# Kernel tuning notes

Hardware: AMD Instinct MI355X
Metric: run time of the kernel (lower is better)

The kernel has to match this reference:

```python
import jax, jax.numpy as jnp
import numpy as np

B, S, E = 4, 1024, 1024
H = 16
HD = E // H  # 64
NEXP = 8
FF = 4 * E
EPS = 1e-5


def _ln(x, g, b):
    m = jnp.mean(x, axis=-1, keepdims=True)
    v = jnp.var(x, axis=-1, keepdims=True)
    return (x - m) * jax.lax.rsqrt(v + EPS) * g + b


def setup_inputs() -> dict:
    key = jax.random.key(0)
    ks = jax.random.split(key, 16)
    sd = 0.02
    inp = {
        "x": jax.random.normal(ks[0], (B, S, E), jnp.float32),
        # per-head Q/K/V linears, stacked over heads: [H, E, HD]
        "wq": jax.random.normal(ks[1], (H, E, HD), jnp.float32) * sd,
        "bq": jnp.zeros((H, HD), jnp.float32),
        "wk": jax.random.normal(ks[2], (H, E, HD), jnp.float32) * sd,
        "bk": jnp.zeros((H, HD), jnp.float32),
        "wv": jax.random.normal(ks[3], (H, E, HD), jnp.float32) * sd,
        "bv": jnp.zeros((H, HD), jnp.float32),
        "wp": jax.random.normal(ks[4], (E, E), jnp.float32) * sd,
        "bp": jnp.zeros((E,), jnp.float32),
        "ln1_g": jnp.ones((E,), jnp.float32),
        "ln1_b": jnp.zeros((E,), jnp.float32),
        "ln2_g": jnp.ones((E,), jnp.float32),
        "ln2_b": jnp.zeros((E,), jnp.float32),
        "wr": jax.random.normal(ks[5], (E, NEXP), jnp.float32) * sd,
        "br": jnp.zeros((NEXP,), jnp.float32),
        # experts stacked: [NEXP, E, FF], [NEXP, FF, E]
        "w1": jax.random.normal(ks[6], (NEXP, E, FF), jnp.float32) * sd,
        "b1": jnp.zeros((NEXP, FF), jnp.float32),
        "w2": jax.random.normal(ks[7], (NEXP, FF, E), jnp.float32) * sd,
        "b2": jnp.zeros((NEXP, E), jnp.float32),
    }
    return inp


def _block(x, wq, bq, wk, bk, wv, bv, wp, bp, ln1_g, ln1_b, ln2_g, ln2_b,
           wr, br, w1, b1, w2, b2):
    # --- multi-head causal attention (per-head Q/K/V, concat, project) ---
    q = jnp.einsum('bse,hed->bhsd', x, wq) + bq[None, :, None, :]
    k = jnp.einsum('bse,hed->bhsd', x, wk) + bk[None, :, None, :]
    v = jnp.einsum('bse,hed->bhsd', x, wv) + bv[None, :, None, :]
    scores = jnp.einsum('bhsd,bhtd->bhst', q, k) / jnp.sqrt(jnp.float32(HD))
    causal = jnp.tril(jnp.ones((S, S), bool))
    scores = jnp.where(causal[None, None], scores, -jnp.inf)
    attn = jax.nn.softmax(scores, axis=-1)
    heads = jnp.einsum('bhst,bhtd->bhsd', attn, v)
    # concat heads (dim order matches torch.cat over head list)
    cat = heads.transpose(0, 2, 1, 3).reshape(B, S, E)
    attn_out = cat @ wp + bp
    # --- residual + LN1 ---
    h = _ln(attn_out + x, ln1_g, ln1_b)
    # --- MoE: router probs weight ALL experts densely (indices unused) ---
    probs = jax.nn.softmax(h @ wr + br, axis=-1)  # [B,S,NEXP]
    mid = jax.nn.relu(jnp.einsum('bse,nef->bnsf', h, w1) + b1[None, :, None, :])
    eo = jnp.einsum('bnsf,nfe->bnse', mid, w2) + b2[None, :, None, :]
    moe_out = jnp.einsum('bnse,bsn->bse', eo, probs)
    # --- residual uses ORIGINAL inputs (as in source) + LN2 ---
    return _ln(moe_out + x, ln2_g, ln2_b)


def reference(x, wq, bq, wk, bk, wv, bv, wp, bp, ln1_g, ln1_b, ln2_g, ln2_b,
              wr, br, w1, b1, w2, b2):
    return _block(x, wq, bq, wk, bk, wv, bv, wp, bp, ln1_g, ln1_b,
                  ln2_g, ln2_b, wr, br, w1, b1, w2, b2)
```

## Files before the change

kernel.cpp:

```cpp
#include <hip/hip_runtime.h>
#include <hip/hip_bf16.h>

typedef unsigned short u16;
typedef unsigned int u32;
typedef __attribute__((ext_vector_type(8))) short bf16x8;
typedef __attribute__((ext_vector_type(4))) float f32x4;

#define DEV static __device__ __forceinline__

DEV u16 f2b(float f) {
  union { float f; u32 u; } v; v.f = f;
  return (u16)((v.u + 0x7fffu + ((v.u >> 16) & 1u)) >> 16);
}

DEV void gload16(const void* g, void* l) {
  __builtin_amdgcn_global_load_lds(
      (const __attribute__((address_space(1))) u32*)g,
      (__attribute__((address_space(3))) u32*)l, 16, 0, 0);
}

__global__ __launch_bounds__(256) void cvt_bf16(const float* __restrict__ s,
                                                u16* __restrict__ d) {
  const long i = ((long)blockIdx.x * 256 + threadIdx.x) * 4;
  const float4 v = *(const float4*)&s[i];
  ushort4 o;
  o.x = f2b(v.x); o.y = f2b(v.y); o.z = f2b(v.z); o.w = f2b(v.w);
  *(ushort4*)&d[i] = o;
}

__global__ __launch_bounds__(256) void tpose_bf16(const float* __restrict__ src,
                                                  u16* __restrict__ dst, int R,
                                                  int C, long sStride,
                                                  long dStride) {
  __shared__ float tl[32][33];
  const float* s = src + (long)blockIdx.z * sStride;
  u16* d = dst + (long)blockIdx.z * dStride;
  const int c0 = blockIdx.x * 32, r0 = blockIdx.y * 32;
  const int tx = threadIdx.x, ty = threadIdx.y;
#pragma unroll
  for (int k = 0; k < 4; k++)
    tl[ty + k * 8][tx] = s[(long)(r0 + ty + k * 8) * C + c0 + tx];
  __syncthreads();
#pragma unroll
  for (int k = 0; k < 4; k++)
    d[(long)(c0 + ty + k * 8) * R + r0 + tx] = f2b(tl[tx][ty + k * 8]);
}

enum { EQKV, EPROJ, EFF1, EFF2, EFF2I };

template <int EPI>
__global__ __launch_bounds__(256, 2) void gemm_bt(
    const u16* __restrict__ A, const u16* __restrict__ Bt, int K, int lda,
    int ldb, const float* __restrict__ c0, const float* __restrict__ c1,
    const float* __restrict__ c2, const float* __restrict__ aux,
    float* __restrict__ fout, u16* __restrict__ o0, u16* __restrict__ o1,
    u16* __restrict__ o2, int nexp) {
  __shared__ u16 As[4096], Bs[4096];
  if constexpr (EPI == EFF2 || EPI == EFF2I) {
    const int z = blockIdx.z;
    A += (long)z * 2048;
    Bt += (long)z * 2048;
    fout += (long)z * 4194304;
  }
  const int tid = threadIdx.x;
  const int m0 = blockIdx.y * 128, n0 = blockIdx.x * 128;
  const int w = tid >> 6, l = tid & 63;
  const int wm = (w >> 1) * 64, wn = (w & 1) * 64;
  const int lr = l & 15, lh = l >> 4;
  f32x4 acc[4][4] = {};
  const u16* Ag = A + (long)(m0 + (tid >> 2)) * lda + (tid & 3) * 8;
  const u16* Bg = Bt + (long)(n0 + (tid >> 2)) * ldb + (tid & 3) * 8;
  const long rsA = (long)64 * lda, rsB = (long)64 * ldb;
  for (int kt = 0; kt < K; kt += 32) {
    __syncthreads();
    gload16(Ag, As + tid * 8);
    gload16(Ag + rsA, As + tid * 8 + 2048);
    gload16(Bg, Bs + tid * 8);
    gload16(Bg + rsB, Bs + tid * 8 + 2048);
    Ag += 32; Bg += 32;
    __syncthreads();
    bf16x8 af[4], bfr[4];
#pragma unroll
    for (int i = 0; i < 4; i++)
      af[i] = *(const bf16x8*)&As[(wm + i * 16 + lr) * 32 + lh * 8];
#pragma unroll
    for (int j = 0; j < 4; j++)
      bfr[j] = *(const bf16x8*)&Bs[(wn + j * 16 + lr) * 32 + lh * 8];
#pragma unroll
    for (int i = 0; i < 4; i++)
#pragma unroll
      for (int j = 0; j < 4; j++)
        acc[i][j] = __builtin_amdgcn_mfma_f32_16x16x32_bf16(af[i], bfr[j],
                                                            acc[i][j], 0, 0, 0);
  }
#pragma unroll
  for (int j = 0; j < 4; j++) {
    const int col = n0 + wn + j * 16 + lr;
#pragma unroll
    for (int i = 0; i < 4; i++)
#pragma unroll
      for (int r = 0; r < 4; r++) {
        const int row = m0 + wm + i * 16 + lh * 4 + r;
        float v = acc[i][j][r];
        if constexpr (EPI == EQKV) {
          const int which = col >> 10, hd = col & 1023;
          const float vb =
              v + ((which == 0) ? c0 : (which == 1) ? c1 : c2)[hd];
          const int b = row >> 10, s = row & 1023;
          const int h = hd >> 6, d = hd & 63;
          const long bh = b * 16 + h;
          if (which == 0)
            o0[(bh * 1024 + s) * 64 + d] = f2b(vb * 0.125f);
          else if (which == 1)
            o1[(bh * 1024 + s) * 64 + d] = f2b(vb);
          else
            o2[bh * 65536 + (long)d * 1024 + s] = f2b(vb);
        } else if constexpr (EPI == EPROJ) {
          const long idx = (long)row * 1024 + col;
          fout[idx] = v + c0[col] + aux[idx];
        } else if constexpr (EPI == EFF1) {
          const float t = v + c0[col];
          o0[(long)row * 4096 + col] = f2b(t > 0.f ? t : 0.f);
        } else {
          float vb = v;
          if (blockIdx.z == 0) vb += c0[col];
          const float t = aux[row * 8 + nexp] * vb;
          const long idx = (long)row * 1024 + col;
          if constexpr (EPI == EFF2I)
            fout[idx] = t;
          else
            fout[idx] = fout[idx] + t;
        }
      }
  }
}

__global__ __launch_bounds__(256) void attn_fwd(const u16* __restrict__ Qb,
                                                const u16* __restrict__ Kb,
                                                const u16* __restrict__ Vt,
                                                u16* __restrict__ Cat) {
  __shared__ u16 Pl[4][512];
  const int tid = threadIdx.x;
  const int w = tid >> 6, l = tid & 63;
  const int lr = l & 15, lh = l >> 4;
  const int bh = blockIdx.y;
  const int q0 = blockIdx.x * 64 + w * 16;
  const u16* Qp = Qb + (long)bh * 65536;
  const u16* Kp = Kb + (long)bh * 65536;
  const u16* Vp = Vt + (long)bh * 65536;
  const bf16x8 qf0 = *(const bf16x8*)&Qp[(q0 + lr) * 64 + lh * 8];
  const bf16x8 qf1 = *(const bf16x8*)&Qp[(q0 + lr) * 64 + 32 + lh * 8];
  f32x4 o[4] = {};
  float mrow[4] = {-1e30f, -1e30f, -1e30f, -1e30f};
  float ssum[4] = {0.f, 0.f, 0.f, 0.f};
  u16* P = Pl[w];
  const int nkt = (q0 + 15) / 32 + 1;
  for (int kt = 0; kt < nkt; kt++) {
    const int t0 = kt * 32;
    f32x4 sc[2];
#pragma unroll
    for (int ts = 0; ts < 2; ts++) {
      const bf16x8 kf0 =
          *(const bf16x8*)&Kp[(t0 + ts * 16 + lr) * 64 + lh * 8];
      const bf16x8 kf1 =
          *(const bf16x8*)&Kp[(t0 + ts * 16 + lr) * 64 + 32 + lh * 8];
      f32x4 c = {};
      c = __builtin_amdgcn_mfma_f32_16x16x32_bf16(qf0, kf0, c, 0, 0, 0);
      c = __builtin_amdgcn_mfma_f32_16x16x32_bf16(qf1, kf1, c, 0, 0, 0);
      sc[ts] = c;
    }
#pragma unroll
    for (int ts = 0; ts < 2; ts++) {
      const int tcol = t0 + ts * 16 + lr;
#pragma unroll
      for (int i = 0; i < 4; i++)
        if (tcol > q0 + lh * 4 + i) sc[ts][i] = -1e30f;
    }
    float mt[4], mnew[4], scl[4], ps[4];
#pragma unroll
    for (int i = 0; i < 4; i++) mt[i] = fmaxf(sc[0][i], sc[1][i]);
#pragma unroll
    for (int d = 1; d < 16; d <<= 1)
#pragma unroll
      for (int i = 0; i < 4; i++) mt[i] = fmaxf(mt[i], __shfl_xor(mt[i], d));
#pragma unroll
    for (int i = 0; i < 4; i++) {
      mnew[i] = fmaxf(mrow[i], mt[i]);
      scl[i] = __expf(mrow[i] - mnew[i]);
      mrow[i] = mnew[i];
      ps[i] = 0.f;
    }
#pragma unroll
    for (int ts = 0; ts < 2; ts++)
#pragma unroll
      for (int i = 0; i < 4; i++) {
        const float p = __expf(sc[ts][i] - mnew[i]);
        ps[i] += p;
        P[(lh * 4 + i) * 32 + ts * 16 + lr] = f2b(p);
      }
#pragma unroll
    for (int d = 1; d < 16; d <<= 1)
#pragma unroll
      for (int i = 0; i < 4; i++) ps[i] += __shfl_xor(ps[i], d);
#pragma unroll
    for (int i = 0; i < 4; i++) ssum[i] = ssum[i] * scl[i] + ps[i];
#pragma unroll
    for (int dt = 0; dt < 4; dt++)
#pragma unroll
      for (int i = 0; i < 4; i++) o[dt][i] *= scl[i];
    const bf16x8 pf = *(const bf16x8*)&P[lr * 32 + lh * 8];
#pragma unroll
    for (int dt = 0; dt < 4; dt++) {
      const bf16x8 vf =
          *(const bf16x8*)&Vp[(dt * 16 + lr) * 1024 + t0 + lh * 8];
      o[dt] = __builtin_amdgcn_mfma_f32_16x16x32_bf16(pf, vf, o[dt], 0, 0, 0);
    }
  }
  const int b = bh >> 4, h = bh & 15;
#pragma unroll
  for (int dt = 0; dt < 4; dt++)
#pragma unroll
    for (int i = 0; i < 4; i++) {
      const int q = q0 + lh * 4 + i;
      Cat[((long)(b * 1024 + q)) * 1024 + h * 64 + dt * 16 + lr] =
          f2b(o[dt][i] / ssum[i]);
    }
}

DEV float wred(float v) {
#pragma unroll
  for (int d = 1; d < 64; d <<= 1) v += __shfl_xor(v, d);
  return v;
}

__global__ __launch_bounds__(256) void ln1_router(
    const float* __restrict__ in, const float* __restrict__ g,
    const float* __restrict__ bb, const float* __restrict__ wr,
    const float* __restrict__ br, u16* __restrict__ h,
    float* __restrict__ probs) {
  __shared__ float rs[4], rs2[4], rp[4][8];
  const int row = blockIdx.x, t = threadIdx.x;
  const int w = t >> 6, l = t & 63;
  const float4 v = *(const float4*)&in[(long)row * 1024 + t * 4];
  float s = v.x + v.y + v.z + v.w;
  float s2 = v.x * v.x + v.y * v.y + v.z * v.z + v.w * v.w;
  s = wred(s);
  s2 = wred(s2);
  if (l == 0) { rs[w] = s; rs2[w] = s2; }
  __syncthreads();
  const float S = rs[0] + rs[1] + rs[2] + rs[3];
  const float S2 = rs2[0] + rs2[1] + rs2[2] + rs2[3];
  const float mean = S * (1.f / 1024.f);
  const float var = S2 * (1.f / 1024.f) - mean * mean;
  const float rr = rsqrtf(var + 1e-5f);
  const float4 gv = *(const float4*)&g[t * 4];
  const float4 bv = *(const float4*)&bb[t * 4];
  float hv[4];
  hv[0] = (v.x - mean) * rr * gv.x + bv.x;
  hv[1] = (v.y - mean) * rr * gv.y + bv.y;
  hv[2] = (v.z - mean) * rr * gv.z + bv.z;
  hv[3] = (v.w - mean) * rr * gv.w + bv.w;
  ushort4 hb;
  hb.x = f2b(hv[0]); hb.y = f2b(hv[1]); hb.z = f2b(hv[2]); hb.w = f2b(hv[3]);
  *(ushort4*)&h[(long)row * 1024 + t * 4] = hb;
  float pr[8] = {};
  const float* wrp = wr + t * 4 * 8;
#pragma unroll
  for (int e = 0; e < 4; e++)
#pragma unroll
    for (int j = 0; j < 8; j++) pr[j] += hv[e] * wrp[e * 8 + j];
#pragma unroll
  for (int j = 0; j < 8; j++) pr[j] = wred(pr[j]);
  if (l == 0)
#pragma unroll
    for (int j = 0; j < 8; j++) rp[w][j] = pr[j];
  __syncthreads();
  if (t == 0) {
    float lg[8], mx = -1e30f;
#pragma unroll
    for (int j = 0; j < 8; j++) {
      lg[j] = rp[0][j] + rp[1][j] + rp[2][j] + rp[3][j] + br[j];
      mx = fmaxf(mx, lg[j]);
    }
    float sm = 0.f;
#pragma unroll
    for (int j = 0; j < 8; j++) {
      lg[j] = __expf(lg[j] - mx);
      sm += lg[j];
    }
    const float inv = 1.f / sm;
#pragma unroll
    for (int j = 0; j < 8; j++) probs[row * 8 + j] = lg[j] * inv;
  }
}

__global__ __launch_bounds__(256) void ln2_kernel(
    const float* __restrict__ in0, const float* __restrict__ in1,
    const float* __restrict__ xres, const float* __restrict__ g,
    const float* __restrict__ bb, float* __restrict__ out) {
  __shared__ float rs[4], rs2[4];
  const int row = blockIdx.x, t = threadIdx.x;
  const int w = t >> 6, l = t & 63;
  const long base = (long)row * 1024 + t * 4;
  const float4 a = *(const float4*)&in0[base];
  const float4 b = *(const float4*)&in1[base];
  const float4 c = *(const float4*)&xres[base];
  float4 v;
  v.x = a.x + b.x + c.x; v.y = a.y + b.y + c.y;
  v.z = a.z + b.z + c.z; v.w = a.w + b.w + c.w;
  float s = v.x + v.y + v.z + v.w;
  float s2 = v.x * v.x + v.y * v.y + v.z * v.z + v.w * v.w;
  s = wred(s);
  s2 = wred(s2);
  if (l == 0) { rs[w] = s; rs2[w] = s2; }
  __syncthreads();
  const float S = rs[0] + rs[1] + rs[2] + rs[3];
  const float S2 = rs2[0] + rs2[1] + rs2[2] + rs2[3];
  const float mean = S * (1.f / 1024.f);
  const float var = S2 * (1.f / 1024.f) - mean * mean;
  const float rr = rsqrtf(var + 1e-5f);
  const float4 gv = *(const float4*)&g[t * 4];
  const float4 bv = *(const float4*)&bb[t * 4];
  float4 o;
  o.x = (v.x - mean) * rr * gv.x + bv.x;
  o.y = (v.y - mean) * rr * gv.y + bv.y;
  o.z = (v.z - mean) * rr * gv.z + bv.z;
  o.w = (v.w - mean) * rr * gv.w + bv.w;
  *(float4*)&out[base] = o;
}

extern "C" void kernel_launch(void* const* d_in, const int* in_sizes, int n_in,
                              void* d_out, int out_size, void* d_ws,
                              size_t ws_size, hipStream_t stream) {
  const float* x = (const float*)d_in[0];
  const float* wq = (const float*)d_in[1];
  const float* bq = (const float*)d_in[2];
  const float* wk = (const float*)d_in[3];
  const float* bk = (const float*)d_in[4];
  const float* wv = (const float*)d_in[5];
  const float* bv = (const float*)d_in[6];
  const float* wp = (const float*)d_in[7];
  const float* bp = (const float*)d_in[8];
  const float* g1 = (const float*)d_in[9];
  const float* be1 = (const float*)d_in[10];
  const float* g2 = (const float*)d_in[11];
  const float* be2 = (const float*)d_in[12];
  const float* wr = (const float*)d_in[13];
  const float* br = (const float*)d_in[14];
  const float* w1 = (const float*)d_in[15];
  const float* b1 = (const float*)d_in[16];
  const float* w2 = (const float*)d_in[17];
  const float* b2 = (const float*)d_in[18];
  float* out = (float*)d_out;

  char* p = (char*)d_ws;
  auto alloc = [&](size_t bytes) {
    char* r = p;
    p += (bytes + 255) & ~(size_t)255;
    return r;
  };
  u16* xb = (u16*)alloc(8388608);
  u16* wqkvt = (u16*)alloc(6291456);
  u16* wpt = (u16*)alloc(2097152);
  u16* w1t = (u16*)alloc(67108864);
  u16* w2t = (u16*)alloc(67108864);
  u16* qb = (u16*)alloc(8388608);
  u16* kb = (u16*)alloc(8388608);
  u16* vt = (u16*)alloc(8388608);
  u16* cat = (u16*)alloc(8388608);
  float* resid1 = (float*)alloc(16777216);
  u16* hb = (u16*)alloc(8388608);
  float* probs = (float*)alloc(131072);
  float* moe = (float*)alloc(33554432);
  u16* mid = qb;

  const dim3 tb(32, 8);
  cvt_bf16<<<4096, 256, 0, stream>>>(x, xb);
  tpose_bf16<<<dim3(2, 32, 16), tb, 0, stream>>>(wq, wqkvt, 1024, 64, 65536, 65536);
  tpose_bf16<<<dim3(2, 32, 16), tb, 0, stream>>>(wk, wqkvt + 1048576, 1024, 64, 65536, 65536);
  tpose_bf16<<<dim3(2, 32, 16), tb, 0, stream>>>(wv, wqkvt + 2097152, 1024, 64, 65536, 65536);
  tpose_bf16<<<dim3(32, 32, 1), tb, 0, stream>>>(wp, wpt, 1024, 1024, 0, 0);
  tpose_bf16<<<dim3(128, 32, 8), tb, 0, stream>>>(w1, w1t, 1024, 4096, 4194304, 4194304);
  tpose_bf16<<<dim3(32, 128, 8), tb, 0, stream>>>(w2, w2t, 4096, 1024, 4194304, 4194304);

  gemm_bt<EQKV><<<dim3(24, 32), 256, 0, stream>>>(
      xb, wqkvt, 1024, 1024, 1024, bq, bk, bv, nullptr, nullptr, qb, kb, vt, 0);
  attn_fwd<<<dim3(16, 64), 256, 0, stream>>>(qb, kb, vt, cat);
  gemm_bt<EPROJ><<<dim3(8, 32), 256, 0, stream>>>(
      cat, wpt, 1024, 1024, 1024, bp, nullptr, nullptr, x, resid1, nullptr,
      nullptr, nullptr, 0);
  ln1_router<<<4096, 256, 0, stream>>>(resid1, g1, be1, wr, br, hb, probs);
  for (int n = 0; n < 8; n++) {
    gemm_bt<EFF1><<<dim3(32, 32), 256, 0, stream>>>(
        hb, w1t + (long)n * 4194304, 1024, 1024, 1024, b1 + n * 4096, nullptr,
        nullptr, nullptr, nullptr, mid, nullptr, nullptr, n);
    if (n == 0)
      gemm_bt<EFF2I><<<dim3(8, 32, 2), 256, 0, stream>>>(
          mid, w2t + (long)n * 4194304, 2048, 4096, 4096, b2 + n * 1024,
          nullptr, nullptr, probs, moe, nullptr, nullptr, nullptr, n);
    else
      gemm_bt<EFF2><<<dim3(8, 32, 2), 256, 0, stream>>>(
          mid, w2t + (long)n * 4194304, 2048, 4096, 4096, b2 + n * 1024,
          nullptr, nullptr, probs, moe, nullptr, nullptr, nullptr, n);
  }
  ln2_kernel<<<4096, 256, 0, stream>>>(moe, moe + 4194304, x, g2, be2, out);
}
```

Measured before the change: 1.646 ms.

## Fold router weights into FF1, batch all experts into two GEMMs, rework attention softmax

The router probability is now applied to the ReLU output inside the FF1 epilogue, and the expert-weighted b2 bias is added in the final LN kernel. This lets all 8 experts run as one concatenated-K GEMM (K=32768, split 4 ways) instead of 16 per-expert launches with read-modify-write accumulation into the output. The GEMM K-tile grows from 32 to 64, doubling LDS per block. Attention drops its LDS round trip for P in favour of a transposed MFMA layout with lane shuffles and vectorized stores. A fallback per-expert path is kept for when the workspace is too small for the 256 MB mid buffer.

```diff
diff --git a/kernel.cpp b/kernel.cpp
--- a/kernel.cpp
+++ b/kernel.cpp
@@ -31,7 +31,7 @@
 __global__ __launch_bounds__(256) void tpose_bf16(const float* __restrict__ src,
                                                   u16* __restrict__ dst, int R,
                                                   int C, long sStride,
-                                                  long dStride) {
+                                                  long dStride, long ldd) {
   __shared__ float tl[32][33];
   const float* s = src + (long)blockIdx.z * sStride;
   u16* d = dst + (long)blockIdx.z * dStride;
@@ -43,24 +43,29 @@
   __syncthreads();
 #pragma unroll
   for (int k = 0; k < 4; k++)
-    d[(long)(c0 + ty + k * 8) * R + r0 + tx] = f2b(tl[tx][ty + k * 8]);
+    d[(long)(c0 + ty + k * 8) * ldd + r0 + tx] = f2b(tl[tx][ty + k * 8]);
 }
 
 enum { EQKV, EPROJ, EFF1, EFF2, EFF2I };
 
 template <int EPI>
 __global__ __launch_bounds__(256, 2) void gemm_bt(
-    const u16* __restrict__ A, const u16* __restrict__ Bt, int K, int lda,
-    int ldb, const float* __restrict__ c0, const float* __restrict__ c1,
+    const u16* __restrict__ A, const u16* __restrict__ Bt, int K, long lda,
+    long ldb, const float* __restrict__ c0, const float* __restrict__ c1,
     const float* __restrict__ c2, const float* __restrict__ aux,
     float* __restrict__ fout, u16* __restrict__ o0, u16* __restrict__ o1,
-    u16* __restrict__ o2, int nexp) {
-  __shared__ u16 As[4096], Bs[4096];
+    u16* __restrict__ o2, int ebase, long ldc) {
+  __shared__ u16 As[8192], Bs[8192];
+  long zc = 0;
   if constexpr (EPI == EFF2 || EPI == EFF2I) {
-    const int z = blockIdx.z;
-    A += (long)z * 2048;
-    Bt += (long)z * 2048;
-    fout += (long)z * 4194304;
+    const long z = blockIdx.z;
+    A += z * (long)K;
+    Bt += z * (long)K;
+    fout += z * 4194304;
+  }
+  if constexpr (EPI == EFF1) {
+    Bt += (long)blockIdx.z * 4194304;
+    zc = (long)blockIdx.z * 4096;
   }
   const int tid = threadIdx.x;
   const int m0 = blockIdx.y * 128, n0 = blockIdx.x * 128;
@@ -68,30 +73,36 @@
   const int wm = (w >> 1) * 64, wn = (w & 1) * 64;
   const int lr = l & 15, lh = l >> 4;
   f32x4 acc[4][4] = {};
-  const u16* Ag = A + (long)(m0 + (tid >> 2)) * lda + (tid & 3) * 8;
-  const u16* Bg = Bt + (long)(n0 + (tid >> 2)) * ldb + (tid & 3) * 8;
-  const long rsA = (long)64 * lda, rsB = (long)64 * ldb;
-  for (int kt = 0; kt < K; kt += 32) {
+  const u16* Ag = A + (long)(m0 + (tid >> 3)) * lda + (tid & 7) * 8;
+  const u16* Bg = Bt + (long)(n0 + (tid >> 3)) * ldb + (tid & 7) * 8;
+  for (int kt = 0; kt < K; kt += 64) {
     __syncthreads();
     gload16(Ag, As + tid * 8);
-    gload16(Ag + rsA, As + tid * 8 + 2048);
+    gload16(Ag + 32 * lda, As + tid * 8 + 2048);
+    gload16(Ag + 64 * lda, As + tid * 8 + 4096);
+    gload16(Ag + 96 * lda, As + tid * 8 + 6144);
     gload16(Bg, Bs + tid * 8);
-    gload16(Bg + rsB, Bs + tid * 8 + 2048);
-    Ag += 32; Bg += 32;
+    gload16(Bg + 32 * ldb, Bs + tid * 8 + 2048);
+    gload16(Bg + 64 * ldb, Bs + tid * 8 + 4096);
+    gload16(Bg + 96 * ldb, Bs + tid * 8 + 6144);
+    Ag += 64; Bg += 64;
     __syncthreads();
-    bf16x8 af[4], bfr[4];
-#pragma unroll
-    for (int i = 0; i < 4; i++)
-      af[i] = *(const bf16x8*)&As[(wm + i * 16 + lr) * 32 + lh * 8];
-#pragma unroll
-    for (int j = 0; j < 4; j++)
-      bfr[j] = *(const bf16x8*)&Bs[(wn + j * 16 + lr) * 32 + lh * 8];
-#pragma unroll
-    for (int i = 0; i < 4; i++)
+#pragma unroll
+    for (int kk = 0; kk < 2; kk++) {
+      bf16x8 af[4], bfr[4];
+#pragma unroll
+      for (int i = 0; i < 4; i++)
+        af[i] = *(const bf16x8*)&As[(wm + i * 16 + lr) * 64 + kk * 32 + lh * 8];
 #pragma unroll
       for (int j = 0; j < 4; j++)
-        acc[i][j] = __builtin_amdgcn_mfma_f32_16x16x32_bf16(af[i], bfr[j],
-                                                            acc[i][j], 0, 0, 0);
+        bfr[j] = *(const bf16x8*)&Bs[(wn + j * 16 + lr) * 64 + kk * 32 + lh * 8];
+#pragma unroll
+      for (int i = 0; i < 4; i++)
+#pragma unroll
+        for (int j = 0; j < 4; j++)
+          acc[i][j] = __builtin_amdgcn_mfma_f32_16x16x32_bf16(
+              af[i], bfr[j], acc[i][j], 0, 0, 0);
+    }
   }
 #pragma unroll
   for (int j = 0; j < 4; j++) {
@@ -119,17 +130,17 @@
           const long idx = (long)row * 1024 + col;
           fout[idx] = v + c0[col] + aux[idx];
         } else if constexpr (EPI == EFF1) {
-          const float t = v + c0[col];
-          o0[(long)row * 4096 + col] = f2b(t > 0.f ? t : 0.f);
+          const int e = ebase + blockIdx.z;
+          const float t = v + c0[(long)e * 4096 + col];
+          const float rl = t > 0.f ? t : 0.f;
+          const float pw = aux[(long)row * 8 + e];
+          o0[(long)row * ldc + zc + col] = f2b(rl * pw);
         } else {
-          float vb = v;
-          if (blockIdx.z == 0) vb += c0[col];
-          const float t = aux[row * 8 + nexp] * vb;
           const long idx = (long)row * 1024 + col;
           if constexpr (EPI == EFF2I)
-            fout[idx] = t;
+            fout[idx] = v;
           else
-            fout[idx] = fout[idx] + t;
+            fout[idx] = fout[idx] + v;
         }
       }
   }
@@ -139,7 +150,6 @@
                                                 const u16* __restrict__ Kb,
                                                 const u16* __restrict__ Vt,
                                                 u16* __restrict__ Cat) {
-  __shared__ u16 Pl[4][512];
   const int tid = threadIdx.x;
   const int w = tid >> 6, l = tid & 63;
   const int lr = l & 15, lh = l >> 4;
@@ -150,81 +160,82 @@
   const u16* Vp = Vt + (long)bh * 65536;
   const bf16x8 qf0 = *(const bf16x8*)&Qp[(q0 + lr) * 64 + lh * 8];
   const bf16x8 qf1 = *(const bf16x8*)&Qp[(q0 + lr) * 64 + 32 + lh * 8];
+  const int q = q0 + lr;
   f32x4 o[4] = {};
-  float mrow[4] = {-1e30f, -1e30f, -1e30f, -1e30f};
-  float ssum[4] = {0.f, 0.f, 0.f, 0.f};
-  u16* P = Pl[w];
-  const int nkt = (q0 + 15) / 32 + 1;
+  float m = -1e30f, ssum = 0.f;
+  const int hi = lh >> 1;
+  const int s0 = ((lh & 1) * 2) * 16 + lr;
+  const int s1 = ((lh & 1) * 2 + 1) * 16 + lr;
+  const int nkt = q0 / 32 + 1;
   for (int kt = 0; kt < nkt; kt++) {
     const int t0 = kt * 32;
     f32x4 sc[2];
 #pragma unroll
     for (int ts = 0; ts < 2; ts++) {
-      const bf16x8 kf0 =
-          *(const bf16x8*)&Kp[(t0 + ts * 16 + lr) * 64 + lh * 8];
+      const bf16x8 kf0 = *(const bf16x8*)&Kp[(t0 + ts * 16 + lr) * 64 + lh * 8];
       const bf16x8 kf1 =
           *(const bf16x8*)&Kp[(t0 + ts * 16 + lr) * 64 + 32 + lh * 8];
       f32x4 c = {};
-      c = __builtin_amdgcn_mfma_f32_16x16x32_bf16(qf0, kf0, c, 0, 0, 0);
-      c = __builtin_amdgcn_mfma_f32_16x16x32_bf16(qf1, kf1, c, 0, 0, 0);
+      c = __builtin_amdgcn_mfma_f32_16x16x32_bf16(kf0, qf0, c, 0, 0, 0);
+      c = __builtin_amdgcn_mfma_f32_16x16x32_bf16(kf1, qf1, c, 0, 0, 0);
       sc[ts] = c;
     }
 #pragma unroll
-    for (int ts = 0; ts < 2; ts++) {
-      const int tcol = t0 + ts * 16 + lr;
-#pragma unroll
-      for (int i = 0; i < 4; i++)
-        if (tcol > q0 + lh * 4 + i) sc[ts][i] = -1e30f;
-    }
-    float mt[4], mnew[4], scl[4], ps[4];
-#pragma unroll
-    for (int i = 0; i < 4; i++) mt[i] = fmaxf(sc[0][i], sc[1][i]);
-#pragma unroll
-    for (int d = 1; d < 16; d <<= 1)
-#pragma unroll
-      for (int i = 0; i < 4; i++) mt[i] = fmaxf(mt[i], __shfl_xor(mt[i], d));
-#pragma unroll
-    for (int i = 0; i < 4; i++) {
-      mnew[i] = fmaxf(mrow[i], mt[i]);
-      scl[i] = __expf(mrow[i] - mnew[i]);
-      mrow[i] = mnew[i];
-      ps[i] = 0.f;
-    }
-#pragma unroll
     for (int ts = 0; ts < 2; ts++)
 #pragma unroll
-      for (int i = 0; i < 4; i++) {
-        const float p = __expf(sc[ts][i] - mnew[i]);
-        ps[i] += p;
-        P[(lh * 4 + i) * 32 + ts * 16 + lr] = f2b(p);
-      }
-#pragma unroll
-    for (int d = 1; d < 16; d <<= 1)
-#pragma unroll
-      for (int i = 0; i < 4; i++) ps[i] += __shfl_xor(ps[i], d);
-#pragma unroll
-    for (int i = 0; i < 4; i++) ssum[i] = ssum[i] * scl[i] + ps[i];
+      for (int r = 0; r < 4; r++)
+        if (t0 + ts * 16 + lh * 4 + r > q) sc[ts][r] = -1e30f;
+    float mt = fmaxf(fmaxf(fmaxf(sc[0][0], sc[0][1]), fmaxf(sc[0][2], sc[0][3])),
+                     fmaxf(fmaxf(sc[1][0], sc[1][1]), fmaxf(sc[1][2], sc[1][3])));
+    mt = fmaxf(mt, __shfl_xor(mt, 16));
+    mt = fmaxf(mt, __shfl_xor(mt, 32));
+    const float mnew = fmaxf(m, mt);
+    const float scl = __expf(m - mnew);
+    m = mnew;
+    float p0[4], p1[4], ps = 0.f;
+#pragma unroll
+    for (int r = 0; r < 4; r++) {
+      p0[r] = __expf(sc[0][r] - mnew);
+      p1[r] = __expf(sc[1][r] - mnew);
+      ps += p0[r] + p1[r];
+    }
+    ssum = ssum * scl + ps;
+    u16 pb[8];
+#pragma unroll
+    for (int r = 0; r < 4; r++) {
+      const float a0 = __shfl(p0[r], s0), b0 = __shfl(p1[r], s0);
+      const float a1 = __shfl(p0[r], s1), b1 = __shfl(p1[r], s1);
+      pb[r] = f2b(hi ? b0 : a0);
+      pb[r + 4] = f2b(hi ? b1 : a1);
+    }
 #pragma unroll
     for (int dt = 0; dt < 4; dt++)
 #pragma unroll
-      for (int i = 0; i < 4; i++) o[dt][i] *= scl[i];
-    const bf16x8 pf = *(const bf16x8*)&P[lr * 32 + lh * 8];
+      for (int r = 0; r < 4; r++) o[dt][r] *= scl;
+    const bf16x8 pf = *(const bf16x8*)pb;
+    __builtin_amdgcn_s_setprio(1);
 #pragma unroll
     for (int dt = 0; dt < 4; dt++) {
       const bf16x8 vf =
           *(const bf16x8*)&Vp[(dt * 16 + lr) * 1024 + t0 + lh * 8];
-      o[dt] = __builtin_amdgcn_mfma_f32_16x16x32_bf16(pf, vf, o[dt], 0, 0, 0);
-    }
-  }
+      o[dt] = __builtin_amdgcn_mfma_f32_16x16x32_bf16(vf, pf, o[dt], 0, 0, 0);
+    }
+    __builtin_amdgcn_s_setprio(0);
+  }
+  ssum += __shfl_xor(ssum, 16);
+  ssum += __shfl_xor(ssum, 32);
+  const float inv = 1.f / ssum;
   const int b = bh >> 4, h = bh & 15;
 #pragma unroll
-  for (int dt = 0; dt < 4; dt++)
-#pragma unroll
-    for (int i = 0; i < 4; i++) {
-      const int q = q0 + lh * 4 + i;
-      Cat[((long)(b * 1024 + q)) * 1024 + h * 64 + dt * 16 + lr] =
-          f2b(o[dt][i] / ssum[i]);
-    }
+  for (int dt = 0; dt < 4; dt++) {
+    ushort4 st;
+    st.x = f2b(o[dt][0] * inv);
+    st.y = f2b(o[dt][1] * inv);
+    st.z = f2b(o[dt][2] * inv);
+    st.w = f2b(o[dt][3] * inv);
+    *(ushort4*)&Cat[((long)(b * 1024 + q)) * 1024 + h * 64 + dt * 16 + lh * 4] =
+        st;
+  }
 }
 
 DEV float wred(float v) {
@@ -295,19 +306,26 @@
 }
 
 __global__ __launch_bounds__(256) void ln2_kernel(
-    const float* __restrict__ in0, const float* __restrict__ in1,
-    const float* __restrict__ xres, const float* __restrict__ g,
-    const float* __restrict__ bb, float* __restrict__ out) {
+    const float* __restrict__ moe, const float* __restrict__ xres,
+    const float* __restrict__ probs, const float* __restrict__ b2,
+    const float* __restrict__ g, const float* __restrict__ bb,
+    float* __restrict__ out, int np) {
   __shared__ float rs[4], rs2[4];
   const int row = blockIdx.x, t = threadIdx.x;
   const int w = t >> 6, l = t & 63;
   const long base = (long)row * 1024 + t * 4;
-  const float4 a = *(const float4*)&in0[base];
-  const float4 b = *(const float4*)&in1[base];
-  const float4 c = *(const float4*)&xres[base];
-  float4 v;
-  v.x = a.x + b.x + c.x; v.y = a.y + b.y + c.y;
-  v.z = a.z + b.z + c.z; v.w = a.w + b.w + c.w;
+  float4 v = *(const float4*)&xres[base];
+  for (int z = 0; z < np; z++) {
+    const float4 a = *(const float4*)&moe[(long)z * 4194304 + base];
+    v.x += a.x; v.y += a.y; v.z += a.z; v.w += a.w;
+  }
+#pragma unroll
+  for (int n = 0; n < 8; n++) {
+    const float pw = probs[(long)row * 8 + n];
+    const float4 bv4 = *(const float4*)&b2[n * 1024 + t * 4];
+    v.x += pw * bv4.x; v.y += pw * bv4.y;
+    v.z += pw * bv4.z; v.w += pw * bv4.w;
+  }
   float s = v.x + v.y + v.z + v.w;
   float s2 = v.x * v.x + v.y * v.y + v.z * v.z + v.w * v.w;
   s = wred(s);
@@ -321,12 +339,12 @@
   const float rr = rsqrtf(var + 1e-5f);
   const float4 gv = *(const float4*)&g[t * 4];
   const float4 bv = *(const float4*)&bb[t * 4];
-  float4 o;
-  o.x = (v.x - mean) * rr * gv.x + bv.x;
-  o.y = (v.y - mean) * rr * gv.y + bv.y;
-  o.z = (v.z - mean) * rr * gv.z + bv.z;
-  o.w = (v.w - mean) * rr * gv.w + bv.w;
-  *(float4*)&out[base] = o;
+  float4 oo;
+  oo.x = (v.x - mean) * rr * gv.x + bv.x;
+  oo.y = (v.y - mean) * rr * gv.y + bv.y;
+  oo.z = (v.z - mean) * rr * gv.z + bv.z;
+  oo.w = (v.w - mean) * rr * gv.w + bv.w;
+  *(float4*)&out[base] = oo;
 }
 
 extern "C" void kernel_launch(void* const* d_in, const int* in_sizes, int n_in,
@@ -359,49 +377,64 @@
     p += (bytes + 255) & ~(size_t)255;
     return r;
   };
+  u16* w1t = (u16*)alloc(67108864);
+  u16* w2t2 = (u16*)alloc(67108864);
+  u16* hb = (u16*)alloc(8388608);
+  float* probs = (float*)alloc(131072);
+  float* moe = (float*)alloc(33554432);
+  float* resid1 = (float*)alloc(16777216);
   u16* xb = (u16*)alloc(8388608);
   u16* wqkvt = (u16*)alloc(6291456);
   u16* wpt = (u16*)alloc(2097152);
-  u16* w1t = (u16*)alloc(67108864);
-  u16* w2t = (u16*)alloc(67108864);
   u16* qb = (u16*)alloc(8388608);
   u16* kb = (u16*)alloc(8388608);
   u16* vt = (u16*)alloc(8388608);
   u16* cat = (u16*)alloc(8388608);
-  float* resid1 = (float*)alloc(16777216);
-  u16* hb = (u16*)alloc(8388608);
-  float* probs = (float*)alloc(131072);
-  float* moe = (float*)alloc(33554432);
-  u16* mid = qb;
+  const size_t need_fast = (size_t)((char*)qb - (char*)d_ws) + (size_t)268435456;
+  const bool fast = ws_size >= need_fast;
 
   const dim3 tb(32, 8);
   cvt_bf16<<<4096, 256, 0, stream>>>(x, xb);
-  tpose_bf16<<<dim3(2, 32, 16), tb, 0, stream>>>(wq, wqkvt, 1024, 64, 65536, 65536);
-  tpose_bf16<<<dim3(2, 32, 16), tb, 0, stream>>>(wk, wqkvt + 1048576, 1024, 64, 65536, 65536);
-  tpose_bf16<<<dim3(2, 32, 16), tb, 0, stream>>>(wv, wqkvt + 2097152, 1024, 64, 65536, 65536);
-  tpose_bf16<<<dim3(32, 32, 1), tb, 0, stream>>>(wp, wpt, 1024, 1024, 0, 0);
-  tpose_bf16<<<dim3(128, 32, 8), tb, 0, stream>>>(w1, w1t, 1024, 4096, 4194304, 4194304);
-  tpose_bf16<<<dim3(32, 128, 8), tb, 0, stream>>>(w2, w2t, 4096, 1024, 4194304, 4194304);
+  tpose_bf16<<<dim3(2, 32, 16), tb, 0, stream>>>(wq, wqkvt, 1024, 64, 65536, 65536, 1024);
+  tpose_bf16<<<dim3(2, 32, 16), tb, 0, stream>>>(wk, wqkvt + 1048576, 1024, 64, 65536, 65536, 1024);
+  tpose_bf16<<<dim3(2, 32, 16), tb, 0, stream>>>(wv, wqkvt + 2097152, 1024, 64, 65536, 65536, 1024);
+  tpose_bf16<<<dim3(32, 32, 1), tb, 0, stream>>>(wp, wpt, 1024, 1024, 0, 0, 1024);
+  tpose_bf16<<<dim3(128, 32, 8), tb, 0, stream>>>(w1, w1t, 1024, 4096, 4194304, 4194304, 1024);
+  tpose_bf16<<<dim3(32, 128, 8), tb, 0, stream>>>(w2, w2t2, 4096, 1024, 4194304, 4096, 32768);
 
   gemm_bt<EQKV><<<dim3(24, 32), 256, 0, stream>>>(
-      xb, wqkvt, 1024, 1024, 1024, bq, bk, bv, nullptr, nullptr, qb, kb, vt, 0);
+      xb, wqkvt, 1024, 1024, 1024, bq, bk, bv, nullptr, nullptr, qb, kb, vt,
+      0, 0);
   attn_fwd<<<dim3(16, 64), 256, 0, stream>>>(qb, kb, vt, cat);
   gemm_bt<EPROJ><<<dim3(8, 32), 256, 0, stream>>>(
       cat, wpt, 1024, 1024, 1024, bp, nullptr, nullptr, x, resid1, nullptr,
-      nullptr, nullptr, 0);
+      nullptr, nullptr, 0, 0);
   ln1_router<<<4096, 256, 0, stream>>>(resid1, g1, be1, wr, br, hb, probs);
-  for (int n = 0; n < 8; n++) {
-    gemm_bt<EFF1><<<dim3(32, 32), 256, 0, stream>>>(
-        hb, w1t + (long)n * 4194304, 1024, 1024, 1024, b1 + n * 4096, nullptr,
-        nullptr, nullptr, nullptr, mid, nullptr, nullptr, n);
-    if (n == 0)
-      gemm_bt<EFF2I><<<dim3(8, 32, 2), 256, 0, stream>>>(
-          mid, w2t + (long)n * 4194304, 2048, 4096, 4096, b2 + n * 1024,
-          nullptr, nullptr, probs, moe, nullptr, nullptr, nullptr, n);
-    else
-      gemm_bt<EFF2><<<dim3(8, 32, 2), 256, 0, stream>>>(
-          mid, w2t + (long)n * 4194304, 2048, 4096, 4096, b2 + n * 1024,
-          nullptr, nullptr, probs, moe, nullptr, nullptr, nullptr, n);
-  }
-  ln2_kernel<<<4096, 256, 0, stream>>>(moe, moe + 4194304, x, g2, be2, out);
-}
+
+  if (fast) {
+    u16* mid = qb;
+    gemm_bt<EFF1><<<dim3(32, 32, 8), 256, 0, stream>>>(
+        hb, w1t, 1024, 1024, 1024, b1, nullptr, nullptr, probs, nullptr, mid,
+        nullptr, nullptr, 0, 32768);
+    gemm_bt<EFF2I><<<dim3(8, 32, 4), 256, 0, stream>>>(
+        mid, w2t2, 8192, 32768, 32768, nullptr, nullptr, nullptr, nullptr,
+        moe, nullptr, nullptr, nullptr, 0, 0);
+    ln2_kernel<<<4096, 256, 0, stream>>>(moe, x, probs, b2, g2, be2, out, 4);
+  } else {
+    u16* mid = qb;
+    for (int n = 0; n < 8; n++) {
+      gemm_bt<EFF1><<<dim3(32, 32, 1), 256, 0, stream>>>(
+          hb, w1t + (long)n * 4194304, 1024, 1024, 1024, b1, nullptr, nullptr,
+          probs, nullptr, mid, nullptr, nullptr, n, 4096);
+      if (n == 0)
+        gemm_bt<EFF2I><<<dim3(8, 32, 2), 256, 0, stream>>>(
+            mid, w2t2 + (long)n * 4096, 2048, 4096, 32768, nullptr, nullptr,
+            nullptr, nullptr, moe, nullptr, nullptr, nullptr, 0, 0);
+      else
+        gemm_bt<EFF2><<<dim3(8, 32, 2), 256, 0, stream>>>(
+            mid, w2t2 + (long)n * 4096, 2048, 4096, 32768, nullptr, nullptr,
+            nullptr, nullptr, moe, nullptr, nullptr, nullptr, 0, 0);
+    }
+    ln2_kernel<<<4096, 256, 0, stream>>>(moe, x, probs, b2, g2, be2, out, 2);
+  }
+}
```

Measured after the change: 1.525 ms. 1.08x faster.
